# Kernel optimization log

Hardware: AMD Instinct MI355X
Metric: run time of the kernel (lower is better)

## Reference

```python
import jax, jax.numpy as jnp
import numpy as np

N_HEADS = 8
ATT_DIM = 64


def _pos_enc(x):
    # x: (chan, L, bs, D); sinusoidal PE added along axis -3 (the query/key slot dim)
    L, D = x.shape[-3], x.shape[-1]
    pos = np.arange(L)[:, None].astype(np.float32)
    div = np.exp(np.arange(0, D, 2).astype(np.float32) * (-np.log(10000.0) / D))
    pe = np.zeros((L, 1, D), dtype=np.float32)
    pe[:, 0, 0::2] = np.sin(pos * div)
    pe[:, 0, 1::2] = np.cos(pos * div)
    return x + jnp.asarray(pe)


def setup_inputs() -> dict:
    key = jax.random.key(0)
    ks = jax.random.split(key, 6)
    C, NQ, NK, B, QD, KD = 8, 16, 32, 128, 128, 128
    E = N_HEADS * ATT_DIM  # 512
    OUT = ATT_DIM  # out_dim defaults to attention_dim
    b = np.float32(1.0 / np.sqrt(ATT_DIM))
    bp = np.float32(1.0 / np.sqrt(OUT))
    return {
        "q": jax.random.normal(ks[0], (C, NQ, B, QD), dtype=jnp.float32),
        "k": jax.random.normal(ks[1], (C, NK, B, KD), dtype=jnp.float32),
        "Wq": jax.random.uniform(ks[2], (C, NQ, QD, E), jnp.float32, -b, b),
        "Wk": jax.random.uniform(ks[3], (C, NK, KD, E), jnp.float32, -b, b),
        "Wv": jax.random.uniform(ks[4], (C, NK, KD, E), jnp.float32, -b, b),
        "Wp": jax.random.uniform(ks[5], (C, NQ, E, OUT), jnp.float32, -bp, bp),
    }


def reference(q, k, Wq, Wk, Wv, Wp):
    H, A = N_HEADS, ATT_DIM
    C, NQ, B, _ = q.shape
    NK = k.shape[1]
    inv_temp = jnp.float32(1.0 / np.sqrt(A))
    q_pe = _pos_enc(q)
    k_pe = _pos_enc(k)
    # per-channel grouped QKV projections: (C, N, B, D) x (C, N, D, E) -> (C, N, B, E)
    query = jnp.einsum('cqbd,cqde->cqbe', q_pe, Wq).reshape(C, NQ, B, H, A)
    key_t = jnp.einsum('ckbd,ckde->ckbe', k_pe, Wk).reshape(C, NK, B, H, A)
    value = jnp.einsum('ckbd,ckde->ckbe', k_pe, Wv).reshape(C, NK, B, H, A)
    # attention scores per (channel, batch, head)
    logits = jnp.einsum('cqbha,ckbha->cbhqk', query, key_t) * inv_temp
    attn = jax.nn.softmax(logits, axis=-1)
    # value aggregation (original does broadcast-multiply+sum; einsum is the same math)
    out = jnp.einsum('cbhqk,ckbha->cqbha', attn, value).reshape(C, NQ, B, H * A)
    # per-channel output projection
    return jnp.einsum('cqbe,cqeo->cqbo', out, Wp)
```

## Files before the change

### kernel.cpp

```cpp
#include <hip/hip_runtime.h>

#define C_  8
#define NQ_ 16
#define NK_ 32
#define B_  128
#define D_  128
#define E_  512
#define H_  8
#define A_  64
#define O_  64

typedef __attribute__((ext_vector_type(4))) float f32x4;
typedef __attribute__((ext_vector_type(8))) short bf16x8;
typedef __attribute__((ext_vector_type(4))) short bf16x4;

__device__ __forceinline__ short f2bf(float f) {
    union { float f; unsigned u; } v; v.f = f;
    unsigned r = v.u + 0x7fffu + ((v.u >> 16) & 1u);
    return (short)(r >> 16);
}

__global__ __launch_bounds__(256) void qkv_proj_kernel(
    const float* __restrict__ qin, const float* __restrict__ kin,
    const float* __restrict__ Wq, const float* __restrict__ Wk,
    const float* __restrict__ Wv,
    short* __restrict__ wsq, short* __restrict__ wsk, short* __restrict__ wsv)
{
    __shared__ __align__(16) short Alds[B_][72];
    __shared__ __align__(16) short Blds[128][72];
    __shared__ float pe_buf[D_];

    const int tid   = threadIdx.x;
    const int blk   = blockIdx.x;
    const int e_blk = blk & 3;
    const int unit  = blk >> 2;

    const float* X; const float* W; short* Y; int n; size_t ypitch;
    if (unit < C_ * NQ_) {
        const int c = unit >> 4;
        n = unit & 15;
        X = qin + (size_t)unit * B_ * D_;
        W = Wq  + (size_t)unit * D_ * E_;
        Y = wsq + (size_t)c * B_ * NQ_ * E_ + (size_t)n * E_;
        ypitch = (size_t)NQ_ * E_;
    } else if (unit < C_ * (NQ_ + NK_)) {
        const int u = unit - C_ * NQ_;
        const int c = u >> 5;
        n = u & 31;
        X = kin + (size_t)u * B_ * D_;
        W = Wk  + (size_t)u * D_ * E_;
        Y = wsk + (size_t)c * B_ * NK_ * E_ + (size_t)n * E_;
        ypitch = (size_t)NK_ * E_;
    } else {
        const int u = unit - C_ * (NQ_ + NK_);
        const int c = u >> 5;
        n = u & 31;
        X = kin + (size_t)u * B_ * D_;
        W = Wv  + (size_t)u * D_ * E_;
        Y = wsv + (size_t)c * B_ * NK_ * E_ + (size_t)n * E_;
        ypitch = (size_t)NK_ * E_;
    }

    if (tid < D_) {
        const int d = tid;
        const float freq = expf((float)(d & ~1) * (-9.210340371976184f / (float)D_));
        const float arg  = (float)n * freq;
        pe_buf[d] = (d & 1) ? cosf(arg) : sinf(arg);
    }
    __syncthreads();

    const int wv   = tid >> 6;
    const int lane = tid & 63;
    const int lr   = lane & 15;
    const int quad = lane >> 4;
    const int wrow = (wv >> 1) * 64;
    const int wcol = (wv & 1) * 64;

    f32x4 acc[4][4];
    for (int m = 0; m < 4; ++m)
        for (int nf = 0; nf < 4; ++nf)
            acc[m][nf] = (f32x4){0.f, 0.f, 0.f, 0.f};

    const int e  = tid & 127;
    const int kg = (tid >> 7) * 32;

    for (int k0 = 0; k0 < D_; k0 += 64) {
        f32x4 a_raw[8];
        #pragma unroll
        for (int i = 0; i < 8; ++i) {
            const int id  = tid + 256 * i;
            const int row = id >> 4;
            const int ch  = id & 15;
            a_raw[i] = *(const f32x4*)(X + (size_t)row * D_ + k0 + ch * 4);
        }
        float b_raw[32];
        const float* bsrc = W + (size_t)(k0 + kg) * E_ + e_blk * 128 + e;
        #pragma unroll
        for (int i = 0; i < 32; ++i)
            b_raw[i] = bsrc[(size_t)i * E_];

        #pragma unroll
        for (int i = 0; i < 8; ++i) {
            const int id  = tid + 256 * i;
            const int row = id >> 4;
            const int ch  = id & 15;
            bf16x4 v;
            #pragma unroll
            for (int j = 0; j < 4; ++j)
                v[j] = f2bf(a_raw[i][j] + pe_buf[k0 + ch * 4 + j]);
            *(bf16x4*)&Alds[row][ch * 4] = v;
        }
        #pragma unroll
        for (int i = 0; i < 4; ++i) {
            bf16x8 v;
            #pragma unroll
            for (int j = 0; j < 8; ++j)
                v[j] = f2bf(b_raw[i * 8 + j]);
            *(bf16x8*)&Blds[e][kg + i * 8] = v;
        }
        __syncthreads();

        for (int ks = 0; ks < 2; ++ks) {
            const int kc = ks * 32 + quad * 8;
            bf16x8 af[4], bfr[4];
            for (int m = 0; m < 4; ++m)
                af[m] = *(const bf16x8*)&Alds[wrow + m * 16 + lr][kc];
            for (int nf = 0; nf < 4; ++nf)
                bfr[nf] = *(const bf16x8*)&Blds[wcol + nf * 16 + lr][kc];
            for (int m = 0; m < 4; ++m)
                for (int nf = 0; nf < 4; ++nf)
                    acc[m][nf] = __builtin_amdgcn_mfma_f32_16x16x32_bf16(
                        af[m], bfr[nf], acc[m][nf], 0, 0, 0);
        }
        __syncthreads();
    }

    for (int m = 0; m < 4; ++m)
        for (int nf = 0; nf < 4; ++nf)
            for (int r = 0; r < 4; ++r) {
                const int row = wrow + m * 16 + quad * 4 + r;
                const int col = e_blk * 128 + wcol + nf * 16 + lr;
                Y[(size_t)row * ypitch + col] = f2bf(acc[m][nf][r]);
            }
}

__global__ __launch_bounds__(256) void attn_kernel(
    const short* __restrict__ wsq, const short* __restrict__ wsk,
    const short* __restrict__ wsv, short* __restrict__ wso)
{
    __shared__ __align__(16) short Qs[16][264];
    __shared__ __align__(16) short Ks[32][264];
    __shared__ __align__(16) short Vs[32][258];
    __shared__ __align__(16) short Ps[4][16][40];

    const int tid = threadIdx.x;
    const int blk = blockIdx.x;
    const int hh  = blk & 1;
    const int b   = (blk >> 1) & (B_ - 1);
    const int c   = blk >> 8;

    const short* qb = wsq + ((size_t)(c * B_ + b) * NQ_) * E_ + hh * 256;
    const short* kb = wsk + ((size_t)(c * B_ + b) * NK_) * E_ + hh * 256;
    const short* vb = wsv + ((size_t)(c * B_ + b) * NK_) * E_ + hh * 256;

    {
        const int nloc = tid >> 5;
        const int ch   = tid & 31;
        #pragma unroll
        for (int i = 0; i < 2; ++i) {
            const int nn = nloc + i * 8;
            *(bf16x8*)&Qs[nn][ch * 8] = *(const bf16x8*)(qb + (size_t)nn * E_ + ch * 8);
        }
        #pragma unroll
        for (int i = 0; i < 4; ++i) {
            const int nn = nloc + i * 8;
            *(bf16x8*)&Ks[nn][ch * 8] = *(const bf16x8*)(kb + (size_t)nn * E_ + ch * 8);
        }
        #pragma unroll
        for (int i = 0; i < 4; ++i) {
            const int nn = nloc + i * 8;
            bf16x8 v = *(const bf16x8*)(vb + (size_t)nn * E_ + ch * 8);
            #pragma unroll
            for (int p = 0; p < 4; ++p)
                *(int*)&Vs[nn][ch * 8 + p * 2] = ((const int*)&v)[p];
        }
    }
    __syncthreads();

    const int wv   = tid >> 6;
    const int lane = tid & 63;
    const int lr   = lane & 15;
    const int quad = lane >> 4;
    const int lcol = wv * 64;

    f32x4 sacc0 = (f32x4){0.f, 0.f, 0.f, 0.f};
    f32x4 sacc1 = (f32x4){0.f, 0.f, 0.f, 0.f};
    #pragma unroll
    for (int ks = 0; ks < 2; ++ks) {
        const int kc = lcol + ks * 32 + quad * 8;
        const bf16x8 aq  = *(const bf16x8*)&Qs[lr][kc];
        const bf16x8 bk0 = *(const bf16x8*)&Ks[lr][kc];
        const bf16x8 bk1 = *(const bf16x8*)&Ks[16 + lr][kc];
        sacc0 = __builtin_amdgcn_mfma_f32_16x16x32_bf16(aq, bk0, sacc0, 0, 0, 0);
        sacc1 = __builtin_amdgcn_mfma_f32_16x16x32_bf16(aq, bk1, sacc1, 0, 0, 0);
    }

    float p0[4], p1[4];
    for (int r = 0; r < 4; ++r) {
        const float v0 = sacc0[r] * 0.125f;
        const float v1 = sacc1[r] * 0.125f;
        float m = fmaxf(v0, v1);
        m = fmaxf(m, __shfl_xor(m, 1));
        m = fmaxf(m, __shfl_xor(m, 2));
        m = fmaxf(m, __shfl_xor(m, 4));
        m = fmaxf(m, __shfl_xor(m, 8));
        const float e0 = __expf(v0 - m);
        const float e1 = __expf(v1 - m);
        float s = e0 + e1;
        s += __shfl_xor(s, 1);
        s += __shfl_xor(s, 2);
        s += __shfl_xor(s, 4);
        s += __shfl_xor(s, 8);
        const float inv = 1.0f / s;
        p0[r] = e0 * inv;
        p1[r] = e1 * inv;
    }

    for (int r = 0; r < 4; ++r) {
        Ps[wv][quad * 4 + r][lr]      = f2bf(p0[r]);
        Ps[wv][quad * 4 + r][16 + lr] = f2bf(p1[r]);
    }
    __syncthreads();
    const bf16x8 ap = *(const bf16x8*)&Ps[wv][lr][quad * 8];

    #pragma unroll
    for (int t = 0; t < 4; ++t) {
        bf16x8 bvv;
        #pragma unroll
        for (int j = 0; j < 8; ++j)
            bvv[j] = Vs[quad * 8 + j][lcol + t * 16 + lr];
        f32x4 oacc = (f32x4){0.f, 0.f, 0.f, 0.f};
        oacc = __builtin_amdgcn_mfma_f32_16x16x32_bf16(ap, bvv, oacc, 0, 0, 0);
        for (int r = 0; r < 4; ++r)
            wso[((size_t)(c * NQ_ + quad * 4 + r) * B_ + b) * E_
                + hh * 256 + lcol + t * 16 + lr] = f2bf(oacc[r]);
    }
}

__global__ __launch_bounds__(256) void out_proj_kernel(
    const short* __restrict__ wso, const float* __restrict__ Wp,
    float* __restrict__ out)
{
    __shared__ __align__(16) short Xlds[64][72];
    __shared__ __align__(16) short Wlds[32][72];

    const int tid = threadIdx.x;
    const int blk = blockIdx.x;
    const int cq  = blk >> 2;
    const int bh  = (blk >> 1) & 1;
    const int oh  = blk & 1;

    const short* Xb = wso + (size_t)cq * B_ * E_ + (size_t)bh * 64 * E_;
    const float* Wb = Wp  + (size_t)cq * E_ * O_ + oh * 32;
    float*       Ob = out + (size_t)cq * B_ * O_ + (size_t)bh * 64 * O_ + oh * 32;

    const int wv   = tid >> 6;
    const int lane = tid & 63;
    const int lr   = lane & 15;
    const int quad = lane >> 4;
    const int o    = tid & 31;
    const int kg   = tid >> 5;

    f32x4 acc[2];
    acc[0] = (f32x4){0.f, 0.f, 0.f, 0.f};
    acc[1] = (f32x4){0.f, 0.f, 0.f, 0.f};

    bf16x8 xv[2][2];
    float  wr[2][8];

    auto issue = [&](int s, int buf) {
        const int k0 = s * 64;
        #pragma unroll
        for (int i = 0; i < 2; ++i) {
            const int task = tid + 256 * i;
            xv[buf][i] = *(const bf16x8*)(Xb + (size_t)(task >> 3) * E_ + k0 + (task & 7) * 8);
        }
        #pragma unroll
        for (int j = 0; j < 8; ++j)
            wr[buf][j] = Wb[(size_t)(k0 + kg * 8 + j) * O_ + o];
    };

    issue(0, 0);
    #pragma unroll
    for (int s = 0; s < 8; ++s) {
        const int cb = s & 1;
        if (s < 7) issue(s + 1, cb ^ 1);

        #pragma unroll
        for (int i = 0; i < 2; ++i) {
            const int task = tid + 256 * i;
            *(bf16x8*)&Xlds[task >> 3][(task & 7) * 8] = xv[cb][i];
        }
        bf16x8 wv8;
        #pragma unroll
        for (int j = 0; j < 8; ++j) wv8[j] = f2bf(wr[cb][j]);
        *(bf16x8*)&Wlds[o][kg * 8] = wv8;
        __syncthreads();

        #pragma unroll
        for (int ks = 0; ks < 2; ++ks) {
            const int kc = ks * 32 + quad * 8;
            const bf16x8 af = *(const bf16x8*)&Xlds[wv * 16 + lr][kc];
            #pragma unroll
            for (int nf = 0; nf < 2; ++nf) {
                const bf16x8 bfr = *(const bf16x8*)&Wlds[nf * 16 + lr][kc];
                acc[nf] = __builtin_amdgcn_mfma_f32_16x16x32_bf16(af, bfr, acc[nf], 0, 0, 0);
            }
        }
        __syncthreads();
    }

    #pragma unroll
    for (int nf = 0; nf < 2; ++nf)
        for (int r = 0; r < 4; ++r)
            Ob[(size_t)(wv * 16 + quad * 4 + r) * O_ + nf * 16 + lr] = acc[nf][r];
}

extern "C" void kernel_launch(void* const* d_in, const int* in_sizes, int n_in,
                              void* d_out, int out_size, void* d_ws, size_t ws_size,
                              hipStream_t stream) {
    const float* q  = (const float*)d_in[0];
    const float* k  = (const float*)d_in[1];
    const float* Wq = (const float*)d_in[2];
    const float* Wk = (const float*)d_in[3];
    const float* Wv = (const float*)d_in[4];
    const float* Wp = (const float*)d_in[5];
    float* out = (float*)d_out;

    const size_t sz_q = (size_t)C_ * NQ_ * B_ * E_;
    const size_t sz_k = (size_t)C_ * NK_ * B_ * E_;
    short* wsq = (short*)d_ws;
    short* wsk = wsq + sz_q;
    short* wsv = wsk + sz_k;
    short* wso = wsv + sz_k;

    qkv_proj_kernel<<<dim3(2560), dim3(256), 0, stream>>>(q, k, Wq, Wk, Wv, wsq, wsk, wsv);
    attn_kernel<<<dim3(2048), dim3(256), 0, stream>>>(wsq, wsk, wsv, wso);
    out_proj_kernel<<<dim3(512), dim3(256), 0, stream>>>(wso, Wp, out);
}
```

Measured before the change: 246.7 us.

## Compute full E per QKV block and change attention output layout

```diff
diff --git a/kernel.cpp b/kernel.cpp
--- a/kernel.cpp
+++ b/kernel.cpp
@@ -20,29 +20,27 @@
     return (short)(r >> 16);
 }
 
-__global__ __launch_bounds__(256) void qkv_proj_kernel(
+__global__ __launch_bounds__(512) void qkv_proj_kernel(
     const float* __restrict__ qin, const float* __restrict__ kin,
     const float* __restrict__ Wq, const float* __restrict__ Wk,
     const float* __restrict__ Wv,
     short* __restrict__ wsq, short* __restrict__ wsk, short* __restrict__ wsv)
 {
-    __shared__ __align__(16) short Alds[B_][72];
-    __shared__ __align__(16) short Blds[128][72];
+    __shared__ __align__(16) short Alds[B_][40];
+    __shared__ __align__(16) short Blds[E_][40];
     __shared__ float pe_buf[D_];
 
-    const int tid   = threadIdx.x;
-    const int blk   = blockIdx.x;
-    const int e_blk = blk & 3;
-    const int unit  = blk >> 2;
-
-    const float* X; const float* W; short* Y; int n; size_t ypitch;
+    const int tid  = threadIdx.x;
+    const int unit = blockIdx.x;
+
+    const float* X; const float* W; short* Y; int n; size_t bpitch;
     if (unit < C_ * NQ_) {
         const int c = unit >> 4;
         n = unit & 15;
         X = qin + (size_t)unit * B_ * D_;
         W = Wq  + (size_t)unit * D_ * E_;
         Y = wsq + (size_t)c * B_ * NQ_ * E_ + (size_t)n * E_;
-        ypitch = (size_t)NQ_ * E_;
+        bpitch = (size_t)NQ_ * E_;
     } else if (unit < C_ * (NQ_ + NK_)) {
         const int u = unit - C_ * NQ_;
         const int c = u >> 5;
@@ -50,7 +48,7 @@
         X = kin + (size_t)u * B_ * D_;
         W = Wk  + (size_t)u * D_ * E_;
         Y = wsk + (size_t)c * B_ * NK_ * E_ + (size_t)n * E_;
-        ypitch = (size_t)NK_ * E_;
+        bpitch = (size_t)NK_ * E_;
     } else {
         const int u = unit - C_ * (NQ_ + NK_);
         const int c = u >> 5;
@@ -58,7 +56,7 @@
         X = kin + (size_t)u * B_ * D_;
         W = Wv  + (size_t)u * D_ * E_;
         Y = wsv + (size_t)c * B_ * NK_ * E_ + (size_t)n * E_;
-        ypitch = (size_t)NK_ * E_;
+        bpitch = (size_t)NK_ * E_;
     }
 
     if (tid < D_) {
@@ -73,74 +71,77 @@
     const int lane = tid & 63;
     const int lr   = lane & 15;
     const int quad = lane >> 4;
-    const int wrow = (wv >> 1) * 64;
-    const int wcol = (wv & 1) * 64;
-
-    f32x4 acc[4][4];
+    const int wrow = (wv >> 2) * 64;
+    const int wcol = (wv & 3) * 128;
+
+    f32x4 acc[4][8];
+    #pragma unroll
     for (int m = 0; m < 4; ++m)
-        for (int nf = 0; nf < 4; ++nf)
+        #pragma unroll
+        for (int nf = 0; nf < 8; ++nf)
             acc[m][nf] = (f32x4){0.f, 0.f, 0.f, 0.f};
 
-    const int e  = tid & 127;
-    const int kg = (tid >> 7) * 32;
-
-    for (int k0 = 0; k0 < D_; k0 += 64) {
-        f32x4 a_raw[8];
-        #pragma unroll
-        for (int i = 0; i < 8; ++i) {
-            const int id  = tid + 256 * i;
-            const int row = id >> 4;
-            const int ch  = id & 15;
-            a_raw[i] = *(const f32x4*)(X + (size_t)row * D_ + k0 + ch * 4);
+    for (int k0 = 0; k0 < D_; k0 += 32) {
+        f32x4 a_raw[2];
+        #pragma unroll
+        for (int i = 0; i < 2; ++i) {
+            const int id  = tid + 512 * i;
+            const int row = id >> 3;
+            const int seg = id & 7;
+            a_raw[i] = *(const f32x4*)(X + (size_t)row * D_ + k0 + seg * 4);
         }
         float b_raw[32];
-        const float* bsrc = W + (size_t)(k0 + kg) * E_ + e_blk * 128 + e;
-        #pragma unroll
-        for (int i = 0; i < 32; ++i)
-            b_raw[i] = bsrc[(size_t)i * E_];
-
-        #pragma unroll
-        for (int i = 0; i < 8; ++i) {
-            const int id  = tid + 256 * i;
-            const int row = id >> 4;
-            const int ch  = id & 15;
+        const float* bsrc = W + (size_t)k0 * E_ + tid;
+        #pragma unroll
+        for (int kk = 0; kk < 32; ++kk)
+            b_raw[kk] = bsrc[(size_t)kk * E_];
+
+        #pragma unroll
+        for (int i = 0; i < 2; ++i) {
+            const int id  = tid + 512 * i;
+            const int row = id >> 3;
+            const int seg = id & 7;
             bf16x4 v;
             #pragma unroll
             for (int j = 0; j < 4; ++j)
-                v[j] = f2bf(a_raw[i][j] + pe_buf[k0 + ch * 4 + j]);
-            *(bf16x4*)&Alds[row][ch * 4] = v;
-        }
-        #pragma unroll
-        for (int i = 0; i < 4; ++i) {
+                v[j] = f2bf(a_raw[i][j] + pe_buf[k0 + seg * 4 + j]);
+            *(bf16x4*)&Alds[row][seg * 4] = v;
+        }
+        #pragma unroll
+        for (int g = 0; g < 4; ++g) {
             bf16x8 v;
             #pragma unroll
             for (int j = 0; j < 8; ++j)
-                v[j] = f2bf(b_raw[i * 8 + j]);
-            *(bf16x8*)&Blds[e][kg + i * 8] = v;
+                v[j] = f2bf(b_raw[g * 8 + j]);
+            *(bf16x8*)&Blds[tid][g * 8] = v;
         }
         __syncthreads();
 
-        for (int ks = 0; ks < 2; ++ks) {
-            const int kc = ks * 32 + quad * 8;
-            bf16x8 af[4], bfr[4];
-            for (int m = 0; m < 4; ++m)
-                af[m] = *(const bf16x8*)&Alds[wrow + m * 16 + lr][kc];
-            for (int nf = 0; nf < 4; ++nf)
-                bfr[nf] = *(const bf16x8*)&Blds[wcol + nf * 16 + lr][kc];
-            for (int m = 0; m < 4; ++m)
-                for (int nf = 0; nf < 4; ++nf)
-                    acc[m][nf] = __builtin_amdgcn_mfma_f32_16x16x32_bf16(
-                        af[m], bfr[nf], acc[m][nf], 0, 0, 0);
-        }
+        bf16x8 af[4], bfr[8];
+        #pragma unroll
+        for (int m = 0; m < 4; ++m)
+            af[m] = *(const bf16x8*)&Alds[wrow + m * 16 + lr][quad * 8];
+        #pragma unroll
+        for (int nf = 0; nf < 8; ++nf)
+            bfr[nf] = *(const bf16x8*)&Blds[wcol + nf * 16 + lr][quad * 8];
+        #pragma unroll
+        for (int m = 0; m < 4; ++m)
+            #pragma unroll
+            for (int nf = 0; nf < 8; ++nf)
+                acc[m][nf] = __builtin_amdgcn_mfma_f32_16x16x32_bf16(
+                    af[m], bfr[nf], acc[m][nf], 0, 0, 0);
         __syncthreads();
     }
 
+    #pragma unroll
     for (int m = 0; m < 4; ++m)
-        for (int nf = 0; nf < 4; ++nf)
+        #pragma unroll
+        for (int nf = 0; nf < 8; ++nf)
+            #pragma unroll
             for (int r = 0; r < 4; ++r) {
                 const int row = wrow + m * 16 + quad * 4 + r;
-                const int col = e_blk * 128 + wcol + nf * 16 + lr;
-                Y[(size_t)row * ypitch + col] = f2bf(acc[m][nf][r]);
+                const int col = wcol + nf * 16 + lr;
+                Y[(size_t)row * bpitch + col] = f2bf(acc[m][nf][r]);
             }
 }
 
@@ -242,7 +243,7 @@
         f32x4 oacc = (f32x4){0.f, 0.f, 0.f, 0.f};
         oacc = __builtin_amdgcn_mfma_f32_16x16x32_bf16(ap, bvv, oacc, 0, 0, 0);
         for (int r = 0; r < 4; ++r)
-            wso[((size_t)(c * NQ_ + quad * 4 + r) * B_ + b) * E_
+            wso[((size_t)(c * B_ + b) * NQ_ + quad * 4 + r) * E_
                 + hh * 256 + lcol + t * 16 + lr] = f2bf(oacc[r]);
     }
 }
@@ -251,7 +252,7 @@
     const short* __restrict__ wso, const float* __restrict__ Wp,
     float* __restrict__ out)
 {
-    __shared__ __align__(16) short Xlds[64][72];
+    __shared__ __align__(16) short Xlds[64][520];
     __shared__ __align__(16) short Wlds[32][72];
 
     const int tid = threadIdx.x;
@@ -259,8 +260,11 @@
     const int cq  = blk >> 2;
     const int bh  = (blk >> 1) & 1;
     const int oh  = blk & 1;
-
-    const short* Xb = wso + (size_t)cq * B_ * E_ + (size_t)bh * 64 * E_;
+    const int c   = cq >> 4;
+    const int qn  = cq & 15;
+
+    const short* Xb = wso + ((size_t)(c * B_ + bh * 64) * NQ_ + qn) * E_;
+    const size_t xpitch = (size_t)NQ_ * E_;
     const float* Wb = Wp  + (size_t)cq * E_ * O_ + oh * 32;
     float*       Ob = out + (size_t)cq * B_ * O_ + (size_t)bh * 64 * O_ + oh * 32;
 
@@ -271,36 +275,42 @@
     const int o    = tid & 31;
     const int kg   = tid >> 5;
 
+    {
+        bf16x8 xv[16];
+        #pragma unroll
+        for (int i = 0; i < 16; ++i) {
+            const int task = tid + 256 * i;
+            const int row  = task >> 6;
+            const int ch   = task & 63;
+            xv[i] = *(const bf16x8*)(Xb + (size_t)row * xpitch + ch * 8);
+        }
+        #pragma unroll
+        for (int i = 0; i < 16; ++i) {
+            const int task = tid + 256 * i;
+            *(bf16x8*)&Xlds[task >> 6][(task & 63) * 8] = xv[i];
+        }
+    }
+
     f32x4 acc[2];
     acc[0] = (f32x4){0.f, 0.f, 0.f, 0.f};
     acc[1] = (f32x4){0.f, 0.f, 0.f, 0.f};
 
-    bf16x8 xv[2][2];
-    float  wr[2][8];
-
-    auto issue = [&](int s, int buf) {
+    float wr[2][8];
+    auto issueW = [&](int s, int buf) {
         const int k0 = s * 64;
-        #pragma unroll
-        for (int i = 0; i < 2; ++i) {
-            const int task = tid + 256 * i;
-            xv[buf][i] = *(const bf16x8*)(Xb + (size_t)(task >> 3) * E_ + k0 + (task & 7) * 8);
-        }
         #pragma unroll
         for (int j = 0; j < 8; ++j)
             wr[buf][j] = Wb[(size_t)(k0 + kg * 8 + j) * O_ + o];
     };
 
-    issue(0, 0);
+    issueW(0, 0);
+    __syncthreads();
+
     #pragma unroll
     for (int s = 0; s < 8; ++s) {
         const int cb = s & 1;
-        if (s < 7) issue(s + 1, cb ^ 1);
-
-        #pragma unroll
-        for (int i = 0; i < 2; ++i) {
-            const int task = tid + 256 * i;
-            *(bf16x8*)&Xlds[task >> 3][(task & 7) * 8] = xv[cb][i];
-        }
+        if (s < 7) issueW(s + 1, cb ^ 1);
+
         bf16x8 wv8;
         #pragma unroll
         for (int j = 0; j < 8; ++j) wv8[j] = f2bf(wr[cb][j]);
@@ -309,11 +319,11 @@
 
         #pragma unroll
         for (int ks = 0; ks < 2; ++ks) {
-            const int kc = ks * 32 + quad * 8;
+            const int kc = s * 64 + ks * 32 + quad * 8;
             const bf16x8 af = *(const bf16x8*)&Xlds[wv * 16 + lr][kc];
             #pragma unroll
             for (int nf = 0; nf < 2; ++nf) {
-                const bf16x8 bfr = *(const bf16x8*)&Wlds[nf * 16 + lr][kc];
+                const bf16x8 bfr = *(const bf16x8*)&Wlds[nf * 16 + lr][(kc & 63)];
                 acc[nf] = __builtin_amdgcn_mfma_f32_16x16x32_bf16(af, bfr, acc[nf], 0, 0, 0);
             }
         }
@@ -344,7 +354,7 @@
     short* wsv = wsk + sz_k;
     short* wso = wsv + sz_k;
 
-    qkv_proj_kernel<<<dim3(2560), dim3(256), 0, stream>>>(q, k, Wq, Wk, Wv, wsq, wsk, wsv);
+    qkv_proj_kernel<<<dim3(640), dim3(512), 0, stream>>>(q, k, Wq, Wk, Wv, wsq, wsk, wsv);
     attn_kernel<<<dim3(2048), dim3(256), 0, stream>>>(wsq, wsk, wsv, wso);
     out_proj_kernel<<<dim3(512), dim3(256), 0, stream>>>(wso, Wp, out);
 }
```

Result: slower. 251.8 us (+2.1%).
